# Kernel tuning notes

Measured on AMD Instinct MI355X. Metric: run time of the kernel, lower is better.

The kernel has to match this reference:

```python
import jax, jax.numpy as jnp
import numpy as np

HIDDEN = 768
VOCAB = 30522
EPS = 1e-12


def setup_inputs() -> dict:
    key = jax.random.key(0)
    ks = jax.random.split(key, 8)
    B, S, H, V, NI = 8, 512, HIDDEN, VOCAB, 10
    features = jax.random.normal(ks[0], (B, S, H), dtype=jnp.float32)
    instance_labels = jax.random.randint(ks[1], (B, S), 0, NI, dtype=jnp.int64)
    # learned params
    dense_w = jax.random.normal(ks[2], (H, 2 * H), dtype=jnp.float32) * 0.02  # torch Linear: [out, in]
    dense_b = jnp.zeros((H,), dtype=jnp.float32)
    ln_w = jnp.ones((H,), dtype=jnp.float32)
    ln_b = jnp.zeros((H,), dtype=jnp.float32)
    dec_w = jax.random.normal(ks[3], (V, H), dtype=jnp.float32) * 0.02
    dec_b = jnp.zeros((V,), dtype=jnp.float32)
    return {
        "features": features,
        "dense_w": dense_w,
        "dense_b": dense_b,
        "ln_w": ln_w,
        "ln_b": ln_b,
        "dec_w": dec_w,
        "dec_b": dec_b,
        "instance_labels": instance_labels,
        "num_instances": NI,
    }


def reference(features, dense_w, dense_b, ln_w, ln_b, dec_w, dec_b,
              instance_labels, num_instances):
    # mlm_mask=None branch of RetrievalHeadIndexDemultiplexing.forward
    positional = features[:, :num_instances, :]                 # [B, NI, H]
    labels = jnp.where(instance_labels == -100, 0, instance_labels)  # [B, S]
    # gather positional rep per token: [B, S, H]
    pos_embeds = jnp.take_along_axis(positional, labels[:, :, None], axis=1)
    x = jnp.concatenate([pos_embeds, features], axis=-1)         # [B, S, 2H]
    x = jnp.einsum('bsk,hk->bsh', x, dense_w) + dense_b          # dense
    x = jax.nn.gelu(x, approximate=False)                        # exact erf gelu
    mu = jnp.mean(x, axis=-1, keepdims=True)
    var = jnp.mean(jnp.square(x - mu), axis=-1, keepdims=True)
    x = (x - mu) * jax.lax.rsqrt(var + EPS) * ln_w + ln_b        # LayerNorm
    logits = jnp.einsum('bsh,vh->bsv', x, dec_w) + dec_b         # decoder
    return logits
```

## Files before the change

### kernel.cpp

```cpp
#include <hip/hip_runtime.h>
#include <hip/hip_bf16.h>

constexpr int HD    = 768;
constexpr int K1    = 1536;
constexpr int VOCAB = 30522;
constexpr int VPAD  = 30592;
constexpr int MROWS = 4096;
constexpr int NINST = 10;

typedef __attribute__((ext_vector_type(8))) short short8;
typedef __attribute__((ext_vector_type(4))) float f32x4;

__device__ __forceinline__ unsigned short f2bf(float f) {
    unsigned int x = __float_as_uint(f);
    x += 0x7fffu + ((x >> 16) & 1u);
    return (unsigned short)(x >> 16);
}

__global__ __launch_bounds__(256) void convert_bf16_kernel(
    const float* __restrict__ src, unsigned short* __restrict__ dst,
    long long valid4, long long total4)
{
    for (long long i = (long long)blockIdx.x * 256 + threadIdx.x; i < total4;
         i += (long long)gridDim.x * 256) {
        uint2 o; o.x = 0u; o.y = 0u;
        if (i < valid4) {
            float4 v = ((const float4*)src)[i];
            o.x = (unsigned)f2bf(v.x) | ((unsigned)f2bf(v.y) << 16);
            o.y = (unsigned)f2bf(v.z) | ((unsigned)f2bf(v.w) << 16);
        }
        ((uint2*)dst)[i] = o;
    }
}

__global__ __launch_bounds__(256) void build_x_kernel(
    const float* __restrict__ feat, const int* __restrict__ labels,
    unsigned short* __restrict__ X)
{
    int m = blockIdx.x;
    int b = m >> 9;
    int lab = labels[m];
    if (lab == -100) lab = 0;
    lab = lab < 0 ? 0 : (lab > NINST - 1 ? NINST - 1 : lab);
    const float4* prow = (const float4*)(feat + ((size_t)b * 512 + lab) * HD);
    const float4* frow = (const float4*)(feat + (size_t)m * HD);
    unsigned short* xr = X + (size_t)m * K1;
    for (int c = threadIdx.x; c < 384; c += 256) {
        float4 v = (c < 192) ? prow[c] : frow[c - 192];
        uint2 o;
        o.x = (unsigned)f2bf(v.x) | ((unsigned)f2bf(v.y) << 16);
        o.y = (unsigned)f2bf(v.z) | ((unsigned)f2bf(v.w) << 16);
        *(uint2*)(xr + c * 4) = o;
    }
}

__global__ __launch_bounds__(256) void ln_kernel(
    const float* __restrict__ y, const float* __restrict__ lnw,
    const float* __restrict__ lnb, unsigned short* __restrict__ hidden)
{
    int r = blockIdx.x;
    int tid = threadIdx.x;
    const float* row = y + (size_t)r * HD;
    float v[3];
    float s = 0.f, sq = 0.f;
#pragma unroll
    for (int i = 0; i < 3; ++i) {
        v[i] = row[tid + i * 256];
        s += v[i];
        sq += v[i] * v[i];
    }
    for (int o = 32; o > 0; o >>= 1) {
        s += __shfl_xor(s, o);
        sq += __shfl_xor(sq, o);
    }
    __shared__ float red[8];
    int w = tid >> 6, lane = tid & 63;
    if (lane == 0) { red[w] = s; red[w + 4] = sq; }
    __syncthreads();
    __shared__ float stats[2];
    if (tid == 0) {
        float S = red[0] + red[1] + red[2] + red[3];
        float Q = red[4] + red[5] + red[6] + red[7];
        float mu = S * (1.f / HD);
        float var = Q * (1.f / HD) - mu * mu;
        stats[0] = mu;
        stats[1] = rsqrtf(var + 1e-12f);
    }
    __syncthreads();
    float mu = stats[0], rs = stats[1];
#pragma unroll
    for (int i = 0; i < 3; ++i) {
        int h = tid + i * 256;
        float o = (v[i] - mu) * rs * lnw[h] + lnb[h];
        hidden[(size_t)r * HD + h] = f2bf(o);
    }
}

#define ASYNC16(SRC, DST) __builtin_amdgcn_global_load_lds( \
    (const __attribute__((address_space(1))) void*)(SRC),   \
    (__attribute__((address_space(3))) void*)(DST), 16, 0, 0)

template<int KTILES, int EPI>
__global__ __launch_bounds__(256, 2) void gemm_bt(
    const unsigned short* __restrict__ A, const unsigned short* __restrict__ Bt,
    const float* __restrict__ bias, float* __restrict__ C,
    int lda, int ldb, int ldc, int nvalid)
{
    __shared__ __align__(16) unsigned short smA[128 * 32];
    __shared__ __align__(16) unsigned short smB[128 * 32];

    const int tid  = threadIdx.x;
    const int lane = tid & 63;
    const int w    = tid >> 6;
    const int wr   = (w >> 1) * 64;
    const int wc   = (w & 1) * 64;

    const int nwg = gridDim.x;
    const int cpx = nwg >> 3;
    const int swz = ((int)blockIdx.x & 7) * cpx + ((int)blockIdx.x >> 3);
    const int m0 = (swz & 31) * 128;
    const int n0 = (swz >> 5) * 128;

    const int srow = tid >> 2;
    const int sc8  = (tid & 3) << 3;
    const int fr   = lane & 15;
    const int fk   = (lane >> 4) << 3;

    f32x4 acc[4][4];
#pragma unroll
    for (int i = 0; i < 4; ++i)
#pragma unroll
        for (int j = 0; j < 4; ++j)
            acc[i][j] = f32x4{0.f, 0.f, 0.f, 0.f};

    for (int kt = 0; kt < KTILES; ++kt) {
        const int k0 = kt * 32;
        __syncthreads();
        {
            const unsigned short* a0 = A + (size_t)(m0 + srow) * lda + k0 + sc8;
            const unsigned short* a1 = A + (size_t)(m0 + 64 + srow) * lda + k0 + sc8;
            const unsigned short* b0 = Bt + (size_t)(n0 + srow) * ldb + k0 + sc8;
            const unsigned short* b1 = Bt + (size_t)(n0 + 64 + srow) * ldb + k0 + sc8;
            ASYNC16(a0, smA + tid * 8);
            ASYNC16(a1, smA + 2048 + tid * 8);
            ASYNC16(b0, smB + tid * 8);
            ASYNC16(b1, smB + 2048 + tid * 8);
        }
        __syncthreads();

        short8 af[4], bfr[4];
#pragma unroll
        for (int i = 0; i < 4; ++i)
            af[i] = *(const short8*)(smA + (wr + i * 16 + fr) * 32 + fk);
#pragma unroll
        for (int j = 0; j < 4; ++j)
            bfr[j] = *(const short8*)(smB + (wc + j * 16 + fr) * 32 + fk);
#pragma unroll
        for (int i = 0; i < 4; ++i)
#pragma unroll
            for (int j = 0; j < 4; ++j)
                acc[i][j] = __builtin_amdgcn_mfma_f32_16x16x32_bf16(
                    af[i], bfr[j], acc[i][j], 0, 0, 0);
    }

    const int coln = lane & 15;
    const int rb   = (lane >> 4) << 2;
#pragma unroll
    for (int i = 0; i < 4; ++i) {
        const int mrow = m0 + wr + i * 16 + rb;
#pragma unroll
        for (int j = 0; j < 4; ++j) {
            const int ncol = n0 + wc + j * 16 + coln;
            if (ncol < nvalid) {
                const float bv = bias[ncol];
#pragma unroll
                for (int r = 0; r < 4; ++r) {
                    float v = acc[i][j][r] + bv;
                    if (EPI == 0)
                        v = 0.5f * v * (1.f + erff(v * 0.70710678118654752f));
                    C[(size_t)(mrow + r) * ldc + ncol] = v;
                }
            }
        }
    }
}

extern "C" void kernel_launch(void* const* d_in, const int* in_sizes, int n_in,
                              void* d_out, int out_size, void* d_ws, size_t ws_size,
                              hipStream_t stream)
{
    const float* features = (const float*)d_in[0];
    const float* dense_w  = (const float*)d_in[1];
    const float* dense_b  = (const float*)d_in[2];
    const float* ln_w     = (const float*)d_in[3];
    const float* ln_b     = (const float*)d_in[4];
    const float* dec_w    = (const float*)d_in[5];
    const float* dec_b    = (const float*)d_in[6];
    const int*   labels   = (const int*)d_in[7];

    char* ws = (char*)d_ws;
    unsigned short* X      = (unsigned short*)(ws);
    unsigned short* denseW = (unsigned short*)(ws + 12582912);
    float*          y      = (float*)(ws + 14942208);
    unsigned short* hidden = (unsigned short*)(ws + 27525120);
    unsigned short* decW   = (unsigned short*)(ws + 33816576);

    convert_bf16_kernel<<<2048, 256, 0, stream>>>(
        dec_w, decW, (long long)VOCAB * HD / 4, (long long)VPAD * HD / 4);
    convert_bf16_kernel<<<512, 256, 0, stream>>>(
        dense_w, denseW, (long long)HD * K1 / 4, (long long)HD * K1 / 4);
    build_x_kernel<<<MROWS, 256, 0, stream>>>(features, labels, X);
    gemm_bt<K1 / 32, 0><<<192, 256, 0, stream>>>(
        X, denseW, dense_b, y, K1, K1, HD, HD);
    ln_kernel<<<MROWS, 256, 0, stream>>>(y, ln_w, ln_b, hidden);
    gemm_bt<HD / 32, 1><<<7648, 256, 0, stream>>>(
        hidden, decW, dec_b, (float*)d_out, HD, HD, VOCAB, VOCAB);
}
```

Before: 916.9 us.

## Replace decoder GEMM with 256x256-tile, 4-stage pipelined, swizzled-LDS kernel

The decoder GEMM (4096x30522x768) now runs in a new kernel using 256x256 tiles with 8 waves, a 4-slot LDS ring of async global-to-LDS loads, and an XOR swizzle on LDS columns to avoid bank conflicts. MFMA phases are interleaved with staging of the next tile and run at raised wave priority. The padded vocabulary grows to 30720 so it divides evenly by 256. The workspace is reorganized so the hidden buffer reuses X's space. The larger tiles raise arithmetic intensity and cut redundant operand loads, in exchange for heavier register and LDS use and hand-tuned waitcnt counts that must exactly match the load pattern.

```diff
diff --git a/kernel.cpp b/kernel.cpp
--- a/kernel.cpp
+++ b/kernel.cpp
@@ -4,21 +4,26 @@
 constexpr int HD    = 768;
 constexpr int K1    = 1536;
 constexpr int VOCAB = 30522;
-constexpr int VPAD  = 30592;
+constexpr int VPAD2 = 30720;
 constexpr int MROWS = 4096;
 constexpr int NINST = 10;
 
 typedef __attribute__((ext_vector_type(8))) short short8;
 typedef __attribute__((ext_vector_type(4))) float f32x4;
-
-__device__ __forceinline__ unsigned short f2bf(float f) {
+typedef unsigned short u16;
+
+__device__ __forceinline__ u16 f2bf(float f) {
     unsigned int x = __float_as_uint(f);
     x += 0x7fffu + ((x >> 16) & 1u);
-    return (unsigned short)(x >> 16);
-}
+    return (u16)(x >> 16);
+}
+
+#define ASYNC16(SRC, DST) __builtin_amdgcn_global_load_lds( \
+    (const __attribute__((address_space(1))) void*)(SRC),   \
+    (__attribute__((address_space(3))) void*)(DST), 16, 0, 0)
 
 __global__ __launch_bounds__(256) void convert_bf16_kernel(
-    const float* __restrict__ src, unsigned short* __restrict__ dst,
+    const float* __restrict__ src, u16* __restrict__ dst,
     long long valid4, long long total4)
 {
     for (long long i = (long long)blockIdx.x * 256 + threadIdx.x; i < total4;
@@ -35,7 +40,7 @@
 
 __global__ __launch_bounds__(256) void build_x_kernel(
     const float* __restrict__ feat, const int* __restrict__ labels,
-    unsigned short* __restrict__ X)
+    u16* __restrict__ X)
 {
     int m = blockIdx.x;
     int b = m >> 9;
@@ -44,7 +49,7 @@
     lab = lab < 0 ? 0 : (lab > NINST - 1 ? NINST - 1 : lab);
     const float4* prow = (const float4*)(feat + ((size_t)b * 512 + lab) * HD);
     const float4* frow = (const float4*)(feat + (size_t)m * HD);
-    unsigned short* xr = X + (size_t)m * K1;
+    u16* xr = X + (size_t)m * K1;
     for (int c = threadIdx.x; c < 384; c += 256) {
         float4 v = (c < 192) ? prow[c] : frow[c - 192];
         uint2 o;
@@ -56,7 +61,7 @@
 
 __global__ __launch_bounds__(256) void ln_kernel(
     const float* __restrict__ y, const float* __restrict__ lnw,
-    const float* __restrict__ lnb, unsigned short* __restrict__ hidden)
+    const float* __restrict__ lnb, u16* __restrict__ hidden)
 {
     int r = blockIdx.x;
     int tid = threadIdx.x;
@@ -96,18 +101,14 @@
     }
 }
 
-#define ASYNC16(SRC, DST) __builtin_amdgcn_global_load_lds( \
-    (const __attribute__((address_space(1))) void*)(SRC),   \
-    (__attribute__((address_space(3))) void*)(DST), 16, 0, 0)
-
 template<int KTILES, int EPI>
 __global__ __launch_bounds__(256, 2) void gemm_bt(
-    const unsigned short* __restrict__ A, const unsigned short* __restrict__ Bt,
+    const u16* __restrict__ A, const u16* __restrict__ Bt,
     const float* __restrict__ bias, float* __restrict__ C,
     int lda, int ldb, int ldc, int nvalid)
 {
-    __shared__ __align__(16) unsigned short smA[128 * 32];
-    __shared__ __align__(16) unsigned short smB[128 * 32];
+    __shared__ __align__(16) u16 smA[128 * 32];
+    __shared__ __align__(16) u16 smB[128 * 32];
 
     const int tid  = threadIdx.x;
     const int lane = tid & 63;
@@ -137,10 +138,10 @@
         const int k0 = kt * 32;
         __syncthreads();
         {
-            const unsigned short* a0 = A + (size_t)(m0 + srow) * lda + k0 + sc8;
-            const unsigned short* a1 = A + (size_t)(m0 + 64 + srow) * lda + k0 + sc8;
-            const unsigned short* b0 = Bt + (size_t)(n0 + srow) * ldb + k0 + sc8;
-            const unsigned short* b1 = Bt + (size_t)(n0 + 64 + srow) * ldb + k0 + sc8;
+            const u16* a0 = A + (size_t)(m0 + srow) * lda + k0 + sc8;
+            const u16* a1 = A + (size_t)(m0 + 64 + srow) * lda + k0 + sc8;
+            const u16* b0 = Bt + (size_t)(n0 + srow) * ldb + k0 + sc8;
+            const u16* b1 = Bt + (size_t)(n0 + 64 + srow) * ldb + k0 + sc8;
             ASYNC16(a0, smA + tid * 8);
             ASYNC16(a1, smA + 2048 + tid * 8);
             ASYNC16(b0, smB + tid * 8);
@@ -185,6 +186,129 @@
     }
 }
 
+__global__ __launch_bounds__(512, 2) void gemm2_256(
+    const u16* __restrict__ A, const u16* __restrict__ Bt,
+    const float* __restrict__ bias, float* __restrict__ C)
+{
+    constexpr int KT = 24;
+    __shared__ __align__(16) u16 lds[4][2][8192];
+
+    const int tid  = threadIdx.x;
+    const int lane = tid & 63;
+    const int w    = tid >> 6;
+    const int wr   = w >> 2;
+    const int wc   = w & 3;
+
+    const int nwg = gridDim.x;
+    const int cpx = nwg >> 3;
+    const int swz = ((int)blockIdx.x & 7) * cpx + ((int)blockIdx.x >> 3);
+    const int m0 = (swz & 15) * 256;
+    const int n0 = (swz >> 4) * 256;
+
+    const int srow   = tid >> 2;
+    const int schunk = (tid & 3) * 8;
+    const int sxor   = ((srow & 8) ? 16 : 0) ^ ((srow & 4) ? 8 : 0);
+    const int scol   = schunk ^ sxor;
+    const u16* aS = A  + (size_t)(m0 + srow) * HD + scol;
+    const u16* bS = Bt + (size_t)(n0 + srow) * HD + scol;
+
+    const int fr = lane & 15;
+    const int fk = (lane >> 4) * 8;
+    const int fx = fk ^ ((fr & 8) ? 16 : 0) ^ ((fr & 4) ? 8 : 0);
+    const int wrOff = wr * 128;
+    const int wc64  = wc * 64;
+
+    f32x4 acc[8][4];
+#pragma unroll
+    for (int i = 0; i < 8; ++i)
+#pragma unroll
+        for (int j = 0; j < 4; ++j)
+            acc[i][j] = f32x4{0.f, 0.f, 0.f, 0.f};
+
+    short8 breg[4], areg[4];
+
+#define STAGEH(SLOT, T, J) do {                                              \
+        ASYNC16(aS + (size_t)(J) * (128 * HD) + (T) * 32,                    \
+                &lds[SLOT][0][(J) * 4096 + tid * 8]);                        \
+        ASYNC16(bS + (size_t)(J) * (128 * HD) + (T) * 32,                    \
+                &lds[SLOT][1][(J) * 4096 + tid * 8]);                        \
+    } while (0)
+
+#define BARRIER() asm volatile("s_barrier" ::: "memory")
+
+#define PHASE_MFMA(IOFF)                                                     \
+    asm volatile("s_waitcnt lgkmcnt(0)" ::: "memory");                       \
+    __builtin_amdgcn_sched_barrier(0);                                       \
+    __builtin_amdgcn_s_setprio(1);                                           \
+    _Pragma("unroll")                                                        \
+    for (int i = 0; i < 4; ++i)                                              \
+        _Pragma("unroll")                                                    \
+        for (int j = 0; j < 4; ++j)                                          \
+            acc[(IOFF) + i][j] = __builtin_amdgcn_mfma_f32_16x16x32_bf16(    \
+                areg[i], breg[j], acc[(IOFF) + i][j], 0, 0, 0);              \
+    __builtin_amdgcn_s_setprio(0);
+
+#define TILE(T, STG, CLOSE_ASM, FINAL_BAR) do {                              \
+        const int s_  = (T) & 3;                                             \
+        const u16* ab_ = &lds[s_][0][0];                                     \
+        const u16* bb_ = &lds[s_][1][0];                                     \
+                                            \
+        _Pragma("unroll")                                                    \
+        for (int j = 0; j < 4; ++j)                                          \
+            breg[j] = *(const short8*)(bb_ + (wc64 + j * 16 + fr) * 32 + fx);\
+        _Pragma("unroll")                                                    \
+        for (int i = 0; i < 4; ++i)                                          \
+            areg[i] = *(const short8*)(ab_ + (wrOff + i * 16 + fr) * 32 + fx);\
+        if (STG) STAGEH((T + 3) & 3, (T) + 3, 0);                            \
+        BARRIER();                                                           \
+        PHASE_MFMA(0)                                                        \
+        BARRIER();                                                           \
+                                       \
+        _Pragma("unroll")                                                    \
+        for (int i = 0; i < 4; ++i)                                          \
+            areg[i] = *(const short8*)(ab_ + (wrOff + 64 + i * 16 + fr) * 32 + fx);\
+        if (STG) STAGEH((T + 3) & 3, (T) + 3, 1);                            \
+        BARRIER();                                                           \
+        PHASE_MFMA(4)                                                        \
+        CLOSE_ASM;                                                           \
+        if (FINAL_BAR) BARRIER();                                            \
+    } while (0)
+
+    STAGEH(0, 0, 0); STAGEH(0, 0, 1);
+    STAGEH(1, 1, 0); STAGEH(1, 1, 1);
+    STAGEH(2, 2, 0); STAGEH(2, 2, 1);
+    asm volatile("s_waitcnt vmcnt(8)" ::: "memory");
+    BARRIER();
+
+    for (int t = 0; t < KT - 3; ++t)
+        TILE(t, true, asm volatile("s_waitcnt vmcnt(8)" ::: "memory"), true);
+    TILE(KT - 3, false, asm volatile("s_waitcnt vmcnt(4)" ::: "memory"), true);
+    TILE(KT - 2, false, asm volatile("s_waitcnt vmcnt(0)" ::: "memory"), true);
+    TILE(KT - 1, false, , false);
+
+#undef TILE
+#undef PHASE_MFMA
+#undef BARRIER
+#undef STAGEH
+
+    const int coln = lane & 15;
+    const int rb   = (lane >> 4) << 2;
+#pragma unroll
+    for (int i = 0; i < 8; ++i) {
+        const int mrow = m0 + wrOff + i * 16 + rb;
+#pragma unroll
+        for (int j = 0; j < 4; ++j) {
+            const int ncol = n0 + wc64 + j * 16 + coln;
+            if (ncol < VOCAB) {
+                const float bv = bias[ncol];
+#pragma unroll
+                for (int r = 0; r < 4; ++r)
+                    C[(size_t)(mrow + r) * VOCAB + ncol] = acc[i][j][r] + bv;
+            }
+        }
+    }
+}
+
 extern "C" void kernel_launch(void* const* d_in, const int* in_sizes, int n_in,
                               void* d_out, int out_size, void* d_ws, size_t ws_size,
                               hipStream_t stream)
@@ -199,20 +323,19 @@
     const int*   labels   = (const int*)d_in[7];
 
     char* ws = (char*)d_ws;
-    unsigned short* X      = (unsigned short*)(ws);
-    unsigned short* denseW = (unsigned short*)(ws + 12582912);
-    float*          y      = (float*)(ws + 14942208);
-    unsigned short* hidden = (unsigned short*)(ws + 27525120);
-    unsigned short* decW   = (unsigned short*)(ws + 33816576);
+    u16*   X      = (u16*)(ws);
+    u16*   hidden = (u16*)(ws);
+    u16*   denseW = (u16*)(ws + 12582912);
+    float* y      = (float*)(ws + 14942208);
+    u16*   decW   = (u16*)(ws + 27525120);
 
     convert_bf16_kernel<<<2048, 256, 0, stream>>>(
-        dec_w, decW, (long long)VOCAB * HD / 4, (long long)VPAD * HD / 4);
+        dec_w, decW, (long long)VOCAB * HD / 4, (long long)VPAD2 * HD / 4);
     convert_bf16_kernel<<<512, 256, 0, stream>>>(
         dense_w, denseW, (long long)HD * K1 / 4, (long long)HD * K1 / 4);
     build_x_kernel<<<MROWS, 256, 0, stream>>>(features, labels, X);
     gemm_bt<K1 / 32, 0><<<192, 256, 0, stream>>>(
         X, denseW, dense_b, y, K1, K1, HD, HD);
     ln_kernel<<<MROWS, 256, 0, stream>>>(y, ln_w, ln_b, hidden);
-    gemm_bt<HD / 32, 1><<<7648, 256, 0, stream>>>(
-        hidden, decW, dec_b, (float*)d_out, HD, HD, VOCAB, VOCAB);
-}
+    gemm2_256<<<1920, 512, 0, stream>>>(hidden, decW, dec_b, (float*)d_out);
+}
```

After: 881.9 us. 3.8% less time.
